# Optimization experiments

Hardware: AMD Instinct MI355X
Metric: run time of the kernel (lower is better)

The kernel has to match this reference:

```python
import jax, jax.numpy as jnp
import numpy as np

BASE_ALPHA = 0.1
NUM_ITER = 4


def setup_inputs() -> dict:
    key = jax.random.key(0)
    k1, k2 = jax.random.split(key)
    pred = jax.random.normal(k1, (8, 8192, 3), dtype=jnp.float32)
    partial = jax.random.normal(k2, (8, 2048, 3), dtype=jnp.float32)
    return {"pred": pred, "partial": partial}


def _pairwise_dist(x, y):
    x2 = jnp.sum(x * x, axis=-1)[..., :, None]          # [B, N, 1]
    y2 = jnp.sum(y * y, axis=-1)[..., None, :]          # [B, 1, M]
    xy = jnp.einsum('bnd,bmd->bnm', x, y)               # [B, N, M]
    return jnp.sqrt(jnp.maximum(x2 + y2 - 2.0 * xy, 0.0))


def reference(pred, partial):
    refined = pred
    for _ in range(NUM_ITER):
        dist = _pairwise_dist(refined, partial)          # [B, N, M]
        min_dist = jnp.min(dist, axis=-1)                # [B, N]
        min_idx = jnp.argmin(dist, axis=-1)              # [B, N]
        nearest = jnp.take_along_axis(partial, min_idx[..., None], axis=1)  # [B, N, 3]
        dist_norm = min_dist / (jnp.max(min_dist, axis=-1, keepdims=True) + 1e-6)
        alpha = BASE_ALPHA * (2.0 - dist_norm)           # [B, N]
        refined = refined + alpha[..., None] * (nearest - refined)
    return refined
```

## Files before the change

### kernel.cpp

```cpp
#include <hip/hip_runtime.h>

#define B 8
#define N 8192
#define M 2048
#define NITER 4
#define BASE_ALPHA 0.1f
#define MARGIN 0.005f
#define CAP 16

#define NTHR 1024
#define NPT 32
#define NSPLIT 32
#define JS (M / NSPLIT)
#define JQ (JS / 4)
#define PT 8
#define PPB (NPT * PT)
#define NBLK (B * N / PPB)

#define LTHR 256
#define BPB 32

#define OFF_AUX   (1024 * 1024)
#define OFF_MASK  (1536 * 1024)
#define OFF_CNT   (1792 * 1024)
#define OFF_CANDL (2048 * 1024)
#define OFF_SLOT0 (4096 * 1024)
#define OFF_SLOT1 (4100 * 1024)

typedef float f2 __attribute__((ext_vector_type(2)));

__global__ __launch_bounds__(NTHR, 4) void iter_kernel(const float* __restrict__ pred,
                                                       const float* __restrict__ partial,
                                                       float4* __restrict__ pos4,
                                                       uint2* __restrict__ aux,
                                                       unsigned int* __restrict__ maskbuf,
                                                       unsigned int* __restrict__ gcnt,
                                                       unsigned short* __restrict__ gcand,
                                                       float* __restrict__ slots) {
    __shared__ float4 sX[M / 4], sY[M / 4], sZ[M / 4], sW[M / 4];
    __shared__ float4 sC[M];
    __shared__ float smint[NSPLIT][PPB];
    __shared__ float4 lpos[PPB];
    __shared__ float thrsh[PPB];
    __shared__ unsigned int smask[PPB];
    __shared__ float pmd[PPB];
    __shared__ float redbuf[4];

    const int tid = threadIdx.x;
    const int b = blockIdx.x >> 5;
    const int blk = blockIdx.x & 31;
    const int gp0 = b * N + blk * PPB;

    const float* pa = partial + b * M * 3;
    if (tid < M / 4) {
        int sp = tid & 31, jq = tid >> 5;
        const float* p0 = pa + (sp * JS + jq * 4) * 3;
        float a0 = p0[0], a1 = p0[1],  a2 = p0[2];
        float b0 = p0[3], b1 = p0[4],  b2 = p0[5];
        float c0 = p0[6], c1 = p0[7],  c2 = p0[8];
        float d0 = p0[9], d1 = p0[10], d2 = p0[11];
        float wa = a0 * a0 + a1 * a1 + a2 * a2;
        float wb = b0 * b0 + b1 * b1 + b2 * b2;
        float wc = c0 * c0 + c1 * c1 + c2 * c2;
        float wd = d0 * d0 + d1 * d1 + d2 * d2;
        sX[tid] = make_float4(-2.f * a0, -2.f * b0, -2.f * c0, -2.f * d0);
        sY[tid] = make_float4(-2.f * a1, -2.f * b1, -2.f * c1, -2.f * d1);
        sZ[tid] = make_float4(-2.f * a2, -2.f * b2, -2.f * c2, -2.f * d2);
        sW[tid] = make_float4(wa, wb, wc, wd);
        int j0 = sp * JS + jq * 4;
        sC[j0 + 0] = make_float4(-2.f * a0, -2.f * a1, -2.f * a2, wa);
        sC[j0 + 1] = make_float4(-2.f * b0, -2.f * b1, -2.f * b2, wb);
        sC[j0 + 2] = make_float4(-2.f * c0, -2.f * c1, -2.f * c2, wc);
        sC[j0 + 3] = make_float4(-2.f * d0, -2.f * d1, -2.f * d2, wd);
    }

    if (tid < PPB) {
        const int p = gp0 + tid;
        const float* pp = pred + (unsigned long long)p * 3;
        float rx = pp[0], ry = pp[1], rz = pp[2];
        float w = rx * rx + ry * ry + rz * rz;
        lpos[tid] = make_float4(rx, ry, rz, w);
        pos4[p] = make_float4(rx, ry, rz, w);
    }
    __syncthreads();

    const int split = tid >> 5;
    const int pt = tid & 31;

    f2 sx[PT], sy[PT], sz[PT];
    #pragma unroll
    for (int k = 0; k < PT; ++k) {
        float4 r = lpos[pt + k * NPT];
        sx[k] = (f2){r.x, r.x}; sy[k] = (f2){r.y, r.y}; sz[k] = (f2){r.z, r.z};
    }
    f2 acc[PT];
    #pragma unroll
    for (int k = 0; k < PT; ++k) acc[k] = (f2){3.402823466e+38f, 3.402823466e+38f};

    #pragma unroll 2
    for (int jq = 0; jq < JQ; ++jq) {
        float4 qx = sX[jq * 32 + split], qy = sY[jq * 32 + split];
        float4 qz = sZ[jq * 32 + split], qw = sW[jq * 32 + split];
        f2 qx01 = (f2){qx.x, qx.y}, qx23 = (f2){qx.z, qx.w};
        f2 qy01 = (f2){qy.x, qy.y}, qy23 = (f2){qy.z, qy.w};
        f2 qz01 = (f2){qz.x, qz.y}, qz23 = (f2){qz.z, qz.w};
        f2 qw01 = (f2){qw.x, qw.y}, qw23 = (f2){qw.z, qw.w};
        #pragma unroll
        for (int k = 0; k < PT; ++k) {
            f2 t01 = __builtin_elementwise_fma(sx[k], qx01,
                     __builtin_elementwise_fma(sy[k], qy01,
                     __builtin_elementwise_fma(sz[k], qz01, qw01)));
            f2 t23 = __builtin_elementwise_fma(sx[k], qx23,
                     __builtin_elementwise_fma(sy[k], qy23,
                     __builtin_elementwise_fma(sz[k], qz23, qw23)));
            acc[k] = __builtin_elementwise_min(acc[k],
                     __builtin_elementwise_min(t01, t23));
        }
    }
    #pragma unroll
    for (int k = 0; k < PT; ++k)
        smint[split][pt + k * NPT] = fminf(acc[k].x, acc[k].y);
    __syncthreads();

    if (tid < PPB) {
        float tstar = 3.402823466e+38f;
        #pragma unroll
        for (int s = 0; s < NSPLIT; ++s) tstar = fminf(tstar, smint[s][tid]);
        const float4 f4 = lpos[tid];
        const float md = sqrtf(fmaxf(f4.w + tstar, 0.0f));
        float mdm = md + MARGIN;
        float thr = fmaf(mdm, mdm, -f4.w);
        thrsh[tid] = thr;
        unsigned int mask = 0u;
        #pragma unroll
        for (int s = 0; s < NSPLIT; ++s)
            if (smint[s][tid] <= thr) mask |= (1u << s);
        smask[tid] = mask;
        maskbuf[gp0 + tid] = mask;
    }
    __syncthreads();

    {
        const int lane = tid & 63;
        const int wv = tid >> 6;
        const unsigned long long lmask = (1ull << lane) - 1ull;
        for (int q0 = 0; q0 < 16; ++q0) {
            int q = wv * 16 + q0;
            float4 f4 = lpos[q];
            float thr = thrsh[q];
            unsigned int m = smask[q];
            int cnt = 0;
            unsigned long long cb = (unsigned long long)(gp0 + q) * CAP;
            float bt = 3.402823466e+38f; int bj = 0;
            while (m) {
                int s = __builtin_ctz(m); m &= m - 1;
                int j = s * JS + lane;
                float4 c = sC[j];
                float t = fmaf(f4.x, c.x, fmaf(f4.y, c.y, fmaf(f4.z, c.z, c.w)));
                if (t < bt) { bt = t; bj = j; }
                bool hit = (t <= thr);
                unsigned long long bal = __ballot(hit);
                int pos = cnt + (int)__popcll(bal & lmask);
                if (hit && pos < CAP)
                    gcand[cb + pos] = (unsigned short)j;
                cnt += (int)__popcll(bal);
            }
            #pragma unroll
            for (int o = 32; o > 0; o >>= 1) {
                float to = __shfl_xor(bt, o);
                int jo = __shfl_xor(bj, o);
                if (to < bt || (to == bt && jo < bj)) { bt = to; bj = jo; }
            }
            if (lane == 0) {
                gcnt[gp0 + q] = (unsigned int)cnt;
                float md = sqrtf(fmaxf(f4.w + bt, 0.0f));
                aux[gp0 + q] = make_uint2(__float_as_uint(md), (unsigned int)bj);
                pmd[q] = md;
            }
        }
    }
    __syncthreads();

    if (tid < PPB) {
        float wm = pmd[tid];
        #pragma unroll
        for (int o = 32; o > 0; o >>= 1) wm = fmaxf(wm, __shfl_down(wm, o));
        if ((tid & 63) == 0) redbuf[tid >> 6] = wm;
    }
    __syncthreads();
    if (tid == 0)
        slots[b * BPB + blk] = fmaxf(fmaxf(redbuf[0], redbuf[1]),
                                     fmaxf(redbuf[2], redbuf[3]));
}

__device__ __attribute__((noinline)) void nn_fallback(float x, float y, float z,
                                                      unsigned int mk,
                                                      const float* __restrict__ pa,
                                                      float& bt_out, int& bj_out) {
    float bt = 3.402823466e+38f; int bj = 0;
    unsigned int m = mk;
    while (m) {
        int s = __builtin_ctz(m); m &= m - 1;
        int jb = s * JS;
        for (int jj = 0; jj < JS; ++jj) {
            int j = jb + jj;
            const float* py = pa + j * 3;
            float y0 = py[0], y1 = py[1], y2 = py[2];
            float qx = -2.f * y0, qy = -2.f * y1, qz = -2.f * y2;
            float qw = y0 * y0 + y1 * y1 + y2 * y2;
            float t = fmaf(x, qx, fmaf(y, qy, fmaf(z, qz, qw)));
            if (t < bt) { bt = t; bj = j; }
        }
    }
    bt_out = bt; bj_out = bj;
}

__global__ __launch_bounds__(LTHR) void light_kernel(const float* __restrict__ partial,
                                                     float4* __restrict__ pos4,
                                                     uint2* __restrict__ aux,
                                                     const unsigned int* __restrict__ maskbuf,
                                                     const unsigned int* __restrict__ gcnt,
                                                     const unsigned short* __restrict__ gcand,
                                                     const float* __restrict__ slots_in,
                                                     float* __restrict__ slots_out) {
    __shared__ float redbuf[4];
    __shared__ float mxsh;

    const int tid = threadIdx.x;
    const int p = blockIdx.x * LTHR + tid;
    const int b = p >> 13;
    const int blk = blockIdx.x & 31;
    const float* pa = partial + b * M * 3;

    if (tid < 64) {
        float v = slots_in[b * BPB + (tid & 31)];
        #pragma unroll
        for (int o = 16; o > 0; o >>= 1) v = fmaxf(v, __shfl_xor(v, o));
        if (tid == 0) mxsh = v;
    }
    __syncthreads();

    float4 f = pos4[p];
    uint2 a = aux[p];
    float md = __uint_as_float(a.x);
    unsigned int cnt = gcnt[p];

    const float* py = pa + (int)a.y * 3;
    float y0 = py[0], y1 = py[1], y2 = py[2];
    float inv = 1.0f / (mxsh + 1e-6f);
    float alpha = BASE_ALPHA * (2.0f - md * inv);
    float nx = fmaf(alpha, y0 - f.x, f.x);
    float ny = fmaf(alpha, y1 - f.y, f.y);
    float nz = fmaf(alpha, y2 - f.z, f.z);
    float w = nx * nx + ny * ny + nz * nz;
    pos4[p] = make_float4(nx, ny, nz, w);

    float bt = 3.402823466e+38f; int bj = 0;
    if (cnt <= CAP) {
        const unsigned short* cp = gcand + (unsigned long long)p * CAP;
        for (unsigned int c = 0; c < cnt; ++c) {
            int j = cp[c];
            const float* pj = pa + j * 3;
            float a0 = pj[0], a1 = pj[1], a2 = pj[2];
            float qx = -2.f * a0, qy = -2.f * a1, qz = -2.f * a2;
            float qw = a0 * a0 + a1 * a1 + a2 * a2;
            float t = fmaf(nx, qx, fmaf(ny, qy, fmaf(nz, qz, qw)));
            if (t < bt || (t == bt && j < bj)) { bt = t; bj = j; }
        }
    } else {
        nn_fallback(nx, ny, nz, maskbuf[p], pa, bt, bj);
    }
    float mdn = sqrtf(fmaxf(w + bt, 0.0f));
    aux[p] = make_uint2(__float_as_uint(mdn), (unsigned int)bj);

    float wm = mdn;
    #pragma unroll
    for (int o = 32; o > 0; o >>= 1) wm = fmaxf(wm, __shfl_down(wm, o));
    if ((tid & 63) == 0) redbuf[tid >> 6] = wm;
    __syncthreads();
    if (tid == 0)
        slots_out[b * BPB + blk] = fmaxf(fmaxf(redbuf[0], redbuf[1]),
                                         fmaxf(redbuf[2], redbuf[3]));
}

__global__ __launch_bounds__(LTHR) void final_kernel(const float* __restrict__ partial,
                                                     const float4* __restrict__ pos4,
                                                     const uint2* __restrict__ aux,
                                                     const float* __restrict__ slots,
                                                     float* __restrict__ out) {
    __shared__ float mxsh;
    const int p = blockIdx.x * LTHR + threadIdx.x;
    const int b = p >> 13;
    if (threadIdx.x < 64) {
        float v = slots[b * BPB + (threadIdx.x & 31)];
        #pragma unroll
        for (int o = 16; o > 0; o >>= 1) v = fmaxf(v, __shfl_xor(v, o));
        if (threadIdx.x == 0) mxsh = v;
    }
    __syncthreads();
    float4 f = pos4[p];
    uint2 a = aux[p];
    float md = __uint_as_float(a.x);
    const float* py = partial + ((unsigned long long)(b * M + (int)a.y)) * 3;
    float y0 = py[0], y1 = py[1], y2 = py[2];
    float inv = 1.0f / (mxsh + 1e-6f);
    float alpha = BASE_ALPHA * (2.0f - md * inv);
    float* po = out + (unsigned long long)p * 3;
    po[0] = fmaf(alpha, y0 - f.x, f.x);
    po[1] = fmaf(alpha, y1 - f.y, f.y);
    po[2] = fmaf(alpha, y2 - f.z, f.z);
}

extern "C" void kernel_launch(void* const* d_in, const int* in_sizes, int n_in,
                              void* d_out, int out_size, void* d_ws, size_t ws_size,
                              hipStream_t stream) {
    const float* pred = (const float*)d_in[0];
    const float* partial = (const float*)d_in[1];
    char* ws = (char*)d_ws;
    float4* pos4 = (float4*)ws;
    uint2* aux = (uint2*)(ws + OFF_AUX);
    unsigned int* maskb = (unsigned int*)(ws + OFF_MASK);
    unsigned int* gcnt = (unsigned int*)(ws + OFF_CNT);
    unsigned short* gcand = (unsigned short*)(ws + OFF_CANDL);
    float* slot0 = (float*)(ws + OFF_SLOT0);
    float* slot1 = (float*)(ws + OFF_SLOT1);
    float* out = (float*)d_out;

    hipLaunchKernelGGL(iter_kernel, dim3(NBLK), dim3(NTHR), 0, stream,
                       pred, partial, pos4, aux, maskb, gcnt, gcand, slot0);
    hipLaunchKernelGGL(light_kernel, dim3(B * N / LTHR), dim3(LTHR), 0, stream,
                       partial, pos4, aux, maskb, gcnt, gcand, slot0, slot1);
    hipLaunchKernelGGL(light_kernel, dim3(B * N / LTHR), dim3(LTHR), 0, stream,
                       partial, pos4, aux, maskb, gcnt, gcand, slot1, slot0);
    hipLaunchKernelGGL(light_kernel, dim3(B * N / LTHR), dim3(LTHR), 0, stream,
                       partial, pos4, aux, maskb, gcnt, gcand, slot0, slot1);
    hipLaunchKernelGGL(final_kernel, dim3(B * N / LTHR), dim3(LTHR), 0, stream,
                       partial, pos4, aux, slot1, out);
}
```

Baseline: 99.85 us.

## Store precomputed candidate and winner coordinates to avoid gathers in light kernels

The iteration kernel now writes each candidate's precomputed (-2y, |y|^2) float4 next to its index, plus the winning neighbor's float4, into new workspace buffers. The light and final kernels read these contiguous float4s instead of gathering scattered 3-float partial points and recomputing norms. The per-block max reductions are replaced by shared-memory atomicMax on float bits, which is valid because the distances are non-negative. This adds extra global writes of 16 bytes per candidate in exchange for fewer dependent, uncoalesced loads in the refinement passes.

```diff
diff --git a/kernel.cpp b/kernel.cpp
--- a/kernel.cpp
+++ b/kernel.cpp
@@ -26,6 +26,8 @@
 #define OFF_CANDL (2048 * 1024)
 #define OFF_SLOT0 (4096 * 1024)
 #define OFF_SLOT1 (4100 * 1024)
+#define OFF_WIN   (5120 * 1024)
+#define OFF_CDATA (6144 * 1024)
 
 typedef float f2 __attribute__((ext_vector_type(2)));
 
@@ -36,6 +38,8 @@
                                                        unsigned int* __restrict__ maskbuf,
                                                        unsigned int* __restrict__ gcnt,
                                                        unsigned short* __restrict__ gcand,
+                                                       float4* __restrict__ gwin,
+                                                       float4* __restrict__ gcdata,
                                                        float* __restrict__ slots) {
     __shared__ float4 sX[M / 4], sY[M / 4], sZ[M / 4], sW[M / 4];
     __shared__ float4 sC[M];
@@ -43,13 +47,14 @@
     __shared__ float4 lpos[PPB];
     __shared__ float thrsh[PPB];
     __shared__ unsigned int smask[PPB];
-    __shared__ float pmd[PPB];
-    __shared__ float redbuf[4];
+    __shared__ unsigned int smaxbits;
 
     const int tid = threadIdx.x;
     const int b = blockIdx.x >> 5;
     const int blk = blockIdx.x & 31;
     const int gp0 = b * N + blk * PPB;
+
+    if (tid == 0) smaxbits = 0u;
 
     const float* pa = partial + b * M * 3;
     if (tid < M / 4) {
@@ -161,8 +166,10 @@
                 bool hit = (t <= thr);
                 unsigned long long bal = __ballot(hit);
                 int pos = cnt + (int)__popcll(bal & lmask);
-                if (hit && pos < CAP)
+                if (hit && pos < CAP) {
                     gcand[cb + pos] = (unsigned short)j;
+                    gcdata[cb + pos] = c;
+                }
                 cnt += (int)__popcll(bal);
             }
             #pragma unroll
@@ -175,22 +182,13 @@
                 gcnt[gp0 + q] = (unsigned int)cnt;
                 float md = sqrtf(fmaxf(f4.w + bt, 0.0f));
                 aux[gp0 + q] = make_uint2(__float_as_uint(md), (unsigned int)bj);
-                pmd[q] = md;
+                gwin[gp0 + q] = sC[bj];
+                atomicMax(&smaxbits, __float_as_uint(md));
             }
         }
     }
     __syncthreads();
-
-    if (tid < PPB) {
-        float wm = pmd[tid];
-        #pragma unroll
-        for (int o = 32; o > 0; o >>= 1) wm = fmaxf(wm, __shfl_down(wm, o));
-        if ((tid & 63) == 0) redbuf[tid >> 6] = wm;
-    }
-    __syncthreads();
-    if (tid == 0)
-        slots[b * BPB + blk] = fmaxf(fmaxf(redbuf[0], redbuf[1]),
-                                     fmaxf(redbuf[2], redbuf[3]));
+    if (tid == 0) slots[b * BPB + blk] = __uint_as_float(smaxbits);
 }
 
 __device__ __attribute__((noinline)) void nn_fallback(float x, float y, float z,
@@ -221,10 +219,12 @@
                                                      const unsigned int* __restrict__ maskbuf,
                                                      const unsigned int* __restrict__ gcnt,
                                                      const unsigned short* __restrict__ gcand,
+                                                     float4* __restrict__ gwin,
+                                                     const float4* __restrict__ gcdata,
                                                      const float* __restrict__ slots_in,
                                                      float* __restrict__ slots_out) {
-    __shared__ float redbuf[4];
     __shared__ float mxsh;
+    __shared__ unsigned int smaxbits;
 
     const int tid = threadIdx.x;
     const int p = blockIdx.x * LTHR + tid;
@@ -232,6 +232,7 @@
     const int blk = blockIdx.x & 31;
     const float* pa = partial + b * M * 3;
 
+    if (tid == 0) smaxbits = 0u;
     if (tid < 64) {
         float v = slots_in[b * BPB + (tid & 31)];
         #pragma unroll
@@ -242,11 +243,11 @@
 
     float4 f = pos4[p];
     uint2 a = aux[p];
+    float4 win = gwin[p];
     float md = __uint_as_float(a.x);
     unsigned int cnt = gcnt[p];
 
-    const float* py = pa + (int)a.y * 3;
-    float y0 = py[0], y1 = py[1], y2 = py[2];
+    float y0 = -0.5f * win.x, y1 = -0.5f * win.y, y2 = -0.5f * win.z;
     float inv = 1.0f / (mxsh + 1e-6f);
     float alpha = BASE_ALPHA * (2.0f - md * inv);
     float nx = fmaf(alpha, y0 - f.x, f.x);
@@ -256,36 +257,34 @@
     pos4[p] = make_float4(nx, ny, nz, w);
 
     float bt = 3.402823466e+38f; int bj = 0;
+    float4 bw = win;
     if (cnt <= CAP) {
-        const unsigned short* cp = gcand + (unsigned long long)p * CAP;
+        const unsigned long long cb = (unsigned long long)p * CAP;
         for (unsigned int c = 0; c < cnt; ++c) {
-            int j = cp[c];
-            const float* pj = pa + j * 3;
-            float a0 = pj[0], a1 = pj[1], a2 = pj[2];
-            float qx = -2.f * a0, qy = -2.f * a1, qz = -2.f * a2;
-            float qw = a0 * a0 + a1 * a1 + a2 * a2;
-            float t = fmaf(nx, qx, fmaf(ny, qy, fmaf(nz, qz, qw)));
-            if (t < bt || (t == bt && j < bj)) { bt = t; bj = j; }
+            float4 q4 = gcdata[cb + c];
+            int j = gcand[cb + c];
+            float t = fmaf(nx, q4.x, fmaf(ny, q4.y, fmaf(nz, q4.z, q4.w)));
+            if (t < bt || (t == bt && j < bj)) { bt = t; bj = j; bw = q4; }
         }
     } else {
         nn_fallback(nx, ny, nz, maskbuf[p], pa, bt, bj);
+        const float* py = pa + bj * 3;
+        float b0 = py[0], b1 = py[1], b2 = py[2];
+        bw = make_float4(-2.f * b0, -2.f * b1, -2.f * b2,
+                         b0 * b0 + b1 * b1 + b2 * b2);
     }
     float mdn = sqrtf(fmaxf(w + bt, 0.0f));
     aux[p] = make_uint2(__float_as_uint(mdn), (unsigned int)bj);
-
-    float wm = mdn;
-    #pragma unroll
-    for (int o = 32; o > 0; o >>= 1) wm = fmaxf(wm, __shfl_down(wm, o));
-    if ((tid & 63) == 0) redbuf[tid >> 6] = wm;
-    __syncthreads();
-    if (tid == 0)
-        slots_out[b * BPB + blk] = fmaxf(fmaxf(redbuf[0], redbuf[1]),
-                                         fmaxf(redbuf[2], redbuf[3]));
-}
-
-__global__ __launch_bounds__(LTHR) void final_kernel(const float* __restrict__ partial,
-                                                     const float4* __restrict__ pos4,
+    gwin[p] = bw;
+
+    atomicMax(&smaxbits, __float_as_uint(mdn));
+    __syncthreads();
+    if (tid == 0) slots_out[b * BPB + blk] = __uint_as_float(smaxbits);
+}
+
+__global__ __launch_bounds__(LTHR) void final_kernel(const float4* __restrict__ pos4,
                                                      const uint2* __restrict__ aux,
+                                                     const float4* __restrict__ gwin,
                                                      const float* __restrict__ slots,
                                                      float* __restrict__ out) {
     __shared__ float mxsh;
@@ -300,9 +299,9 @@
     __syncthreads();
     float4 f = pos4[p];
     uint2 a = aux[p];
+    float4 win = gwin[p];
     float md = __uint_as_float(a.x);
-    const float* py = partial + ((unsigned long long)(b * M + (int)a.y)) * 3;
-    float y0 = py[0], y1 = py[1], y2 = py[2];
+    float y0 = -0.5f * win.x, y1 = -0.5f * win.y, y2 = -0.5f * win.z;
     float inv = 1.0f / (mxsh + 1e-6f);
     float alpha = BASE_ALPHA * (2.0f - md * inv);
     float* po = out + (unsigned long long)p * 3;
@@ -324,16 +323,18 @@
     unsigned short* gcand = (unsigned short*)(ws + OFF_CANDL);
     float* slot0 = (float*)(ws + OFF_SLOT0);
     float* slot1 = (float*)(ws + OFF_SLOT1);
+    float4* gwin = (float4*)(ws + OFF_WIN);
+    float4* gcdata = (float4*)(ws + OFF_CDATA);
     float* out = (float*)d_out;
 
     hipLaunchKernelGGL(iter_kernel, dim3(NBLK), dim3(NTHR), 0, stream,
-                       pred, partial, pos4, aux, maskb, gcnt, gcand, slot0);
+                       pred, partial, pos4, aux, maskb, gcnt, gcand, gwin, gcdata, slot0);
     hipLaunchKernelGGL(light_kernel, dim3(B * N / LTHR), dim3(LTHR), 0, stream,
-                       partial, pos4, aux, maskb, gcnt, gcand, slot0, slot1);
+                       partial, pos4, aux, maskb, gcnt, gcand, gwin, gcdata, slot0, slot1);
     hipLaunchKernelGGL(light_kernel, dim3(B * N / LTHR), dim3(LTHR), 0, stream,
-                       partial, pos4, aux, maskb, gcnt, gcand, slot1, slot0);
+                       partial, pos4, aux, maskb, gcnt, gcand, gwin, gcdata, slot1, slot0);
     hipLaunchKernelGGL(light_kernel, dim3(B * N / LTHR), dim3(LTHR), 0, stream,
-                       partial, pos4, aux, maskb, gcnt, gcand, slot0, slot1);
+                       partial, pos4, aux, maskb, gcnt, gcand, gwin, gcdata, slot0, slot1);
     hipLaunchKernelGGL(final_kernel, dim3(B * N / LTHR), dim3(LTHR), 0, stream,
-                       partial, pos4, aux, slot1, out);
-}
+                       pos4, aux, gwin, slot1, out);
+}
```

Measured after the change: 107.5 us. 7.6% more time.

## Fuse all iterations into one cooperative kernel with grid sync and LDS candidates

Applied to the files above, without the earlier changes.

Replaces the five kernel launches (heavy first pass, three light refinement passes, final update) with a single cooperative kernel. Per-point state and candidate lists stay in shared memory across iterations, and grid.sync() handles the per-batch max reduction. The change also drops the separate SoA partial-point arrays and reads the packed sC layout in the main loop. This removes launch overhead and global round trips for positions, candidates and masks, but adds grid-wide barriers and more shared memory per block, and relies on all 256 blocks of 1024 threads being co-resident.

```diff
diff --git a/kernel.cpp b/kernel.cpp
--- a/kernel.cpp
+++ b/kernel.cpp
@@ -1,4 +1,7 @@
 #include <hip/hip_runtime.h>
+#include <hip/hip_cooperative_groups.h>
+
+namespace cg = cooperative_groups;
 
 #define B 8
 #define N 8192
@@ -16,36 +19,28 @@
 #define PT 8
 #define PPB (NPT * PT)
 #define NBLK (B * N / PPB)
-
-#define LTHR 256
 #define BPB 32
 
-#define OFF_AUX   (1024 * 1024)
-#define OFF_MASK  (1536 * 1024)
-#define OFF_CNT   (1792 * 1024)
-#define OFF_CANDL (2048 * 1024)
-#define OFF_SLOT0 (4096 * 1024)
-#define OFF_SLOT1 (4100 * 1024)
 
 typedef float f2 __attribute__((ext_vector_type(2)));
 
-__global__ __launch_bounds__(NTHR, 4) void iter_kernel(const float* __restrict__ pred,
-                                                       const float* __restrict__ partial,
-                                                       float4* __restrict__ pos4,
-                                                       uint2* __restrict__ aux,
-                                                       unsigned int* __restrict__ maskbuf,
-                                                       unsigned int* __restrict__ gcnt,
-                                                       unsigned short* __restrict__ gcand,
-                                                       float* __restrict__ slots) {
-    __shared__ float4 sX[M / 4], sY[M / 4], sZ[M / 4], sW[M / 4];
+__global__ __launch_bounds__(NTHR, 4) void fused_all(const float* __restrict__ pred,
+                                                     const float* __restrict__ partial,
+                                                     float* __restrict__ slots,
+                                                     float* __restrict__ out) {
     __shared__ float4 sC[M];
     __shared__ float smint[NSPLIT][PPB];
     __shared__ float4 lpos[PPB];
     __shared__ float thrsh[PPB];
     __shared__ unsigned int smask[PPB];
-    __shared__ float pmd[PPB];
+    __shared__ unsigned short cc[PPB][CAP];
+    __shared__ unsigned int scnt[PPB];
+    __shared__ unsigned short sidx[PPB];
+    __shared__ float smd[PPB];
     __shared__ float redbuf[4];
-
+    __shared__ float mxsh;
+
+    cg::grid_group grid = cg::this_grid();
     const int tid = threadIdx.x;
     const int b = blockIdx.x >> 5;
     const int blk = blockIdx.x & 31;
@@ -59,28 +54,20 @@
         float b0 = p0[3], b1 = p0[4],  b2 = p0[5];
         float c0 = p0[6], c1 = p0[7],  c2 = p0[8];
         float d0 = p0[9], d1 = p0[10], d2 = p0[11];
-        float wa = a0 * a0 + a1 * a1 + a2 * a2;
-        float wb = b0 * b0 + b1 * b1 + b2 * b2;
-        float wc = c0 * c0 + c1 * c1 + c2 * c2;
-        float wd = d0 * d0 + d1 * d1 + d2 * d2;
-        sX[tid] = make_float4(-2.f * a0, -2.f * b0, -2.f * c0, -2.f * d0);
-        sY[tid] = make_float4(-2.f * a1, -2.f * b1, -2.f * c1, -2.f * d1);
-        sZ[tid] = make_float4(-2.f * a2, -2.f * b2, -2.f * c2, -2.f * d2);
-        sW[tid] = make_float4(wa, wb, wc, wd);
         int j0 = sp * JS + jq * 4;
-        sC[j0 + 0] = make_float4(-2.f * a0, -2.f * a1, -2.f * a2, wa);
-        sC[j0 + 1] = make_float4(-2.f * b0, -2.f * b1, -2.f * b2, wb);
-        sC[j0 + 2] = make_float4(-2.f * c0, -2.f * c1, -2.f * c2, wc);
-        sC[j0 + 3] = make_float4(-2.f * d0, -2.f * d1, -2.f * d2, wd);
-    }
-
+        sC[j0 + 0] = make_float4(-2.f * a0, -2.f * a1, -2.f * a2,
+                                 a0 * a0 + a1 * a1 + a2 * a2);
+        sC[j0 + 1] = make_float4(-2.f * b0, -2.f * b1, -2.f * b2,
+                                 b0 * b0 + b1 * b1 + b2 * b2);
+        sC[j0 + 2] = make_float4(-2.f * c0, -2.f * c1, -2.f * c2,
+                                 c0 * c0 + c1 * c1 + c2 * c2);
+        sC[j0 + 3] = make_float4(-2.f * d0, -2.f * d1, -2.f * d2,
+                                 d0 * d0 + d1 * d1 + d2 * d2);
+    }
     if (tid < PPB) {
-        const int p = gp0 + tid;
-        const float* pp = pred + (unsigned long long)p * 3;
+        const float* pp = pred + (unsigned long long)(gp0 + tid) * 3;
         float rx = pp[0], ry = pp[1], rz = pp[2];
-        float w = rx * rx + ry * ry + rz * rz;
-        lpos[tid] = make_float4(rx, ry, rz, w);
-        pos4[p] = make_float4(rx, ry, rz, w);
+        lpos[tid] = make_float4(rx, ry, rz, rx * rx + ry * ry + rz * rz);
     }
     __syncthreads();
 
@@ -99,12 +86,12 @@
 
     #pragma unroll 2
     for (int jq = 0; jq < JQ; ++jq) {
-        float4 qx = sX[jq * 32 + split], qy = sY[jq * 32 + split];
-        float4 qz = sZ[jq * 32 + split], qw = sW[jq * 32 + split];
-        f2 qx01 = (f2){qx.x, qx.y}, qx23 = (f2){qx.z, qx.w};
-        f2 qy01 = (f2){qy.x, qy.y}, qy23 = (f2){qy.z, qy.w};
-        f2 qz01 = (f2){qz.x, qz.y}, qz23 = (f2){qz.z, qz.w};
-        f2 qw01 = (f2){qw.x, qw.y}, qw23 = (f2){qw.z, qw.w};
+        const int j0 = split * JS + jq * 4;
+        float4 c0 = sC[j0 + 0], c1 = sC[j0 + 1], c2 = sC[j0 + 2], c3 = sC[j0 + 3];
+        f2 qx01 = (f2){c0.x, c1.x}, qx23 = (f2){c2.x, c3.x};
+        f2 qy01 = (f2){c0.y, c1.y}, qy23 = (f2){c2.y, c3.y};
+        f2 qz01 = (f2){c0.z, c1.z}, qz23 = (f2){c2.z, c3.z};
+        f2 qw01 = (f2){c0.w, c1.w}, qw23 = (f2){c2.w, c3.w};
         #pragma unroll
         for (int k = 0; k < PT; ++k) {
             f2 t01 = __builtin_elementwise_fma(sx[k], qx01,
@@ -136,7 +123,6 @@
         for (int s = 0; s < NSPLIT; ++s)
             if (smint[s][tid] <= thr) mask |= (1u << s);
         smask[tid] = mask;
-        maskbuf[gp0 + tid] = mask;
     }
     __syncthreads();
 
@@ -150,7 +136,6 @@
             float thr = thrsh[q];
             unsigned int m = smask[q];
             int cnt = 0;
-            unsigned long long cb = (unsigned long long)(gp0 + q) * CAP;
             float bt = 3.402823466e+38f; int bj = 0;
             while (m) {
                 int s = __builtin_ctz(m); m &= m - 1;
@@ -162,7 +147,7 @@
                 unsigned long long bal = __ballot(hit);
                 int pos = cnt + (int)__popcll(bal & lmask);
                 if (hit && pos < CAP)
-                    gcand[cb + pos] = (unsigned short)j;
+                    cc[q][pos] = (unsigned short)j;
                 cnt += (int)__popcll(bal);
             }
             #pragma unroll
@@ -172,143 +157,94 @@
                 if (to < bt || (to == bt && jo < bj)) { bt = to; bj = jo; }
             }
             if (lane == 0) {
-                gcnt[gp0 + q] = (unsigned int)cnt;
-                float md = sqrtf(fmaxf(f4.w + bt, 0.0f));
-                aux[gp0 + q] = make_uint2(__float_as_uint(md), (unsigned int)bj);
-                pmd[q] = md;
+                scnt[q] = (unsigned int)cnt;
+                smd[q] = sqrtf(fmaxf(f4.w + bt, 0.0f));
+                sidx[q] = (unsigned short)bj;
             }
         }
     }
     __syncthreads();
 
     if (tid < PPB) {
-        float wm = pmd[tid];
+        float wm = smd[tid];
         #pragma unroll
         for (int o = 32; o > 0; o >>= 1) wm = fmaxf(wm, __shfl_down(wm, o));
         if ((tid & 63) == 0) redbuf[tid >> 6] = wm;
     }
     __syncthreads();
     if (tid == 0)
-        slots[b * BPB + blk] = fmaxf(fmaxf(redbuf[0], redbuf[1]),
-                                     fmaxf(redbuf[2], redbuf[3]));
-}
-
-__device__ __attribute__((noinline)) void nn_fallback(float x, float y, float z,
-                                                      unsigned int mk,
-                                                      const float* __restrict__ pa,
-                                                      float& bt_out, int& bj_out) {
-    float bt = 3.402823466e+38f; int bj = 0;
-    unsigned int m = mk;
-    while (m) {
-        int s = __builtin_ctz(m); m &= m - 1;
-        int jb = s * JS;
-        for (int jj = 0; jj < JS; ++jj) {
-            int j = jb + jj;
-            const float* py = pa + j * 3;
-            float y0 = py[0], y1 = py[1], y2 = py[2];
-            float qx = -2.f * y0, qy = -2.f * y1, qz = -2.f * y2;
-            float qw = y0 * y0 + y1 * y1 + y2 * y2;
-            float t = fmaf(x, qx, fmaf(y, qy, fmaf(z, qz, qw)));
-            if (t < bt) { bt = t; bj = j; }
-        }
-    }
-    bt_out = bt; bj_out = bj;
-}
-
-__global__ __launch_bounds__(LTHR) void light_kernel(const float* __restrict__ partial,
-                                                     float4* __restrict__ pos4,
-                                                     uint2* __restrict__ aux,
-                                                     const unsigned int* __restrict__ maskbuf,
-                                                     const unsigned int* __restrict__ gcnt,
-                                                     const unsigned short* __restrict__ gcand,
-                                                     const float* __restrict__ slots_in,
-                                                     float* __restrict__ slots_out) {
-    __shared__ float redbuf[4];
-    __shared__ float mxsh;
-
-    const int tid = threadIdx.x;
-    const int p = blockIdx.x * LTHR + tid;
-    const int b = p >> 13;
-    const int blk = blockIdx.x & 31;
-    const float* pa = partial + b * M * 3;
-
-    if (tid < 64) {
-        float v = slots_in[b * BPB + (tid & 31)];
-        #pragma unroll
-        for (int o = 16; o > 0; o >>= 1) v = fmaxf(v, __shfl_xor(v, o));
-        if (tid == 0) mxsh = v;
-    }
-    __syncthreads();
-
-    float4 f = pos4[p];
-    uint2 a = aux[p];
-    float md = __uint_as_float(a.x);
-    unsigned int cnt = gcnt[p];
-
-    const float* py = pa + (int)a.y * 3;
-    float y0 = py[0], y1 = py[1], y2 = py[2];
-    float inv = 1.0f / (mxsh + 1e-6f);
-    float alpha = BASE_ALPHA * (2.0f - md * inv);
-    float nx = fmaf(alpha, y0 - f.x, f.x);
-    float ny = fmaf(alpha, y1 - f.y, f.y);
-    float nz = fmaf(alpha, y2 - f.z, f.z);
-    float w = nx * nx + ny * ny + nz * nz;
-    pos4[p] = make_float4(nx, ny, nz, w);
-
-    float bt = 3.402823466e+38f; int bj = 0;
-    if (cnt <= CAP) {
-        const unsigned short* cp = gcand + (unsigned long long)p * CAP;
-        for (unsigned int c = 0; c < cnt; ++c) {
-            int j = cp[c];
-            const float* pj = pa + j * 3;
-            float a0 = pj[0], a1 = pj[1], a2 = pj[2];
-            float qx = -2.f * a0, qy = -2.f * a1, qz = -2.f * a2;
-            float qw = a0 * a0 + a1 * a1 + a2 * a2;
-            float t = fmaf(nx, qx, fmaf(ny, qy, fmaf(nz, qz, qw)));
-            if (t < bt || (t == bt && j < bj)) { bt = t; bj = j; }
-        }
-    } else {
-        nn_fallback(nx, ny, nz, maskbuf[p], pa, bt, bj);
-    }
-    float mdn = sqrtf(fmaxf(w + bt, 0.0f));
-    aux[p] = make_uint2(__float_as_uint(mdn), (unsigned int)bj);
-
-    float wm = mdn;
-    #pragma unroll
-    for (int o = 32; o > 0; o >>= 1) wm = fmaxf(wm, __shfl_down(wm, o));
-    if ((tid & 63) == 0) redbuf[tid >> 6] = wm;
-    __syncthreads();
-    if (tid == 0)
-        slots_out[b * BPB + blk] = fmaxf(fmaxf(redbuf[0], redbuf[1]),
-                                         fmaxf(redbuf[2], redbuf[3]));
-}
-
-__global__ __launch_bounds__(LTHR) void final_kernel(const float* __restrict__ partial,
-                                                     const float4* __restrict__ pos4,
-                                                     const uint2* __restrict__ aux,
-                                                     const float* __restrict__ slots,
-                                                     float* __restrict__ out) {
-    __shared__ float mxsh;
-    const int p = blockIdx.x * LTHR + threadIdx.x;
-    const int b = p >> 13;
-    if (threadIdx.x < 64) {
-        float v = slots[b * BPB + (threadIdx.x & 31)];
-        #pragma unroll
-        for (int o = 16; o > 0; o >>= 1) v = fmaxf(v, __shfl_xor(v, o));
-        if (threadIdx.x == 0) mxsh = v;
-    }
-    __syncthreads();
-    float4 f = pos4[p];
-    uint2 a = aux[p];
-    float md = __uint_as_float(a.x);
-    const float* py = partial + ((unsigned long long)(b * M + (int)a.y)) * 3;
-    float y0 = py[0], y1 = py[1], y2 = py[2];
-    float inv = 1.0f / (mxsh + 1e-6f);
-    float alpha = BASE_ALPHA * (2.0f - md * inv);
-    float* po = out + (unsigned long long)p * 3;
-    po[0] = fmaf(alpha, y0 - f.x, f.x);
-    po[1] = fmaf(alpha, y1 - f.y, f.y);
-    po[2] = fmaf(alpha, y2 - f.z, f.z);
+        slots[0 * NBLK + b * BPB + blk] = fmaxf(fmaxf(redbuf[0], redbuf[1]),
+                                                fmaxf(redbuf[2], redbuf[3]));
+    grid.sync();
+
+    for (int u = 1; u <= NITER; ++u) {
+        if (tid < 64) {
+            float v = slots[(u - 1) * NBLK + b * BPB + (tid & 31)];
+            #pragma unroll
+            for (int o = 16; o > 0; o >>= 1) v = fmaxf(v, __shfl_xor(v, o));
+            if (tid == 0) mxsh = v;
+        }
+        __syncthreads();
+
+        if (tid < PPB) {
+            float4 f = lpos[tid];
+            float md = smd[tid];
+            int idx = sidx[tid];
+            float4 q = sC[idx];
+            float y0 = -0.5f * q.x, y1 = -0.5f * q.y, y2 = -0.5f * q.z;
+            float inv = 1.0f / (mxsh + 1e-6f);
+            float alpha = BASE_ALPHA * (2.0f - md * inv);
+            float nx = fmaf(alpha, y0 - f.x, f.x);
+            float ny = fmaf(alpha, y1 - f.y, f.y);
+            float nz = fmaf(alpha, y2 - f.z, f.z);
+            if (u == NITER) {
+                float* po = out + (unsigned long long)(gp0 + tid) * 3;
+                po[0] = nx; po[1] = ny; po[2] = nz;
+            } else {
+                float w = nx * nx + ny * ny + nz * nz;
+                lpos[tid] = make_float4(nx, ny, nz, w);
+                float bt = 3.402823466e+38f; int bj = 0;
+                unsigned int cnt = scnt[tid];
+                if (cnt <= CAP) {
+                    for (unsigned int c = 0; c < cnt; ++c) {
+                        int j = cc[tid][c];
+                        float4 q4 = sC[j];
+                        float t = fmaf(nx, q4.x, fmaf(ny, q4.y, fmaf(nz, q4.z, q4.w)));
+                        if (t < bt || (t == bt && j < bj)) { bt = t; bj = j; }
+                    }
+                } else {
+                    unsigned int m = smask[tid];
+                    while (m) {
+                        int s = __builtin_ctz(m); m &= m - 1;
+                        int jb = s * JS;
+                        for (int jj = 0; jj < JS; ++jj) {
+                            int j = jb + jj;
+                            float4 q4 = sC[j];
+                            float t = fmaf(nx, q4.x, fmaf(ny, q4.y, fmaf(nz, q4.z, q4.w)));
+                            if (t < bt) { bt = t; bj = j; }
+                        }
+                    }
+                }
+                smd[tid] = sqrtf(fmaxf(w + bt, 0.0f));
+                sidx[tid] = (unsigned short)bj;
+            }
+        }
+
+        if (u < NITER) {
+            __syncthreads();
+            if (tid < PPB) {
+                float wm = smd[tid];
+                #pragma unroll
+                for (int o = 32; o > 0; o >>= 1) wm = fmaxf(wm, __shfl_down(wm, o));
+                if ((tid & 63) == 0) redbuf[tid >> 6] = wm;
+            }
+            __syncthreads();
+            if (tid == 0)
+                slots[u * NBLK + b * BPB + blk] = fmaxf(fmaxf(redbuf[0], redbuf[1]),
+                                                        fmaxf(redbuf[2], redbuf[3]));
+            grid.sync();
+        }
+    }
 }
 
 extern "C" void kernel_launch(void* const* d_in, const int* in_sizes, int n_in,
@@ -316,24 +252,10 @@
                               hipStream_t stream) {
     const float* pred = (const float*)d_in[0];
     const float* partial = (const float*)d_in[1];
-    char* ws = (char*)d_ws;
-    float4* pos4 = (float4*)ws;
-    uint2* aux = (uint2*)(ws + OFF_AUX);
-    unsigned int* maskb = (unsigned int*)(ws + OFF_MASK);
-    unsigned int* gcnt = (unsigned int*)(ws + OFF_CNT);
-    unsigned short* gcand = (unsigned short*)(ws + OFF_CANDL);
-    float* slot0 = (float*)(ws + OFF_SLOT0);
-    float* slot1 = (float*)(ws + OFF_SLOT1);
+    float* slots = (float*)d_ws;
     float* out = (float*)d_out;
 
-    hipLaunchKernelGGL(iter_kernel, dim3(NBLK), dim3(NTHR), 0, stream,
-                       pred, partial, pos4, aux, maskb, gcnt, gcand, slot0);
-    hipLaunchKernelGGL(light_kernel, dim3(B * N / LTHR), dim3(LTHR), 0, stream,
-                       partial, pos4, aux, maskb, gcnt, gcand, slot0, slot1);
-    hipLaunchKernelGGL(light_kernel, dim3(B * N / LTHR), dim3(LTHR), 0, stream,
-                       partial, pos4, aux, maskb, gcnt, gcand, slot1, slot0);
-    hipLaunchKernelGGL(light_kernel, dim3(B * N / LTHR), dim3(LTHR), 0, stream,
-                       partial, pos4, aux, maskb, gcnt, gcand, slot0, slot1);
-    hipLaunchKernelGGL(final_kernel, dim3(B * N / LTHR), dim3(LTHR), 0, stream,
-                       partial, pos4, aux, slot1, out);
+    void* args[] = {(void*)&pred, (void*)&partial, (void*)&slots, (void*)&out};
+    hipLaunchCooperativeKernel((const void*)fused_all, dim3(NBLK), dim3(NTHR),
+                               args, 0, stream);
 }
```

After: 201.9 us. 102% more time.
